# Performance work log

Measured on AMD Instinct MI355X. Metric: run time of the kernel, lower is better.

The kernel has to match this reference:

```python
import jax, jax.numpy as jnp
import numpy as np

B, S, H, NH = 4, 2048, 1024, 16
DK = H // NH


def setup_inputs() -> dict:
    key = jax.random.key(0)
    ks = jax.random.split(key, 12)
    sd = 1.0 / np.sqrt(H)
    inp = {
        "query": jax.random.normal(ks[0], (B, S, H), jnp.float32),
        "key_": jax.random.normal(ks[1], (B, S, H), jnp.float32),
        "value": jax.random.normal(ks[2], (B, S, H), jnp.float32),
        "mask": jax.random.randint(ks[3], (B, 1, S, S), 0, 2) == 1,
        "Wq": jax.random.uniform(ks[4], (H, H), jnp.float32, -sd, sd),
        "bq": jnp.zeros((H,), jnp.float32),
        "Wk": jax.random.uniform(ks[5], (H, H), jnp.float32, -sd, sd),
        "bk": jnp.zeros((H,), jnp.float32),
        "Wv": jax.random.uniform(ks[6], (H, H), jnp.float32, -sd, sd),
        "bv": jnp.zeros((H,), jnp.float32),
        "Wo": jax.random.uniform(ks[7], (H, H), jnp.float32, -sd, sd),
        "bo": jnp.zeros((H,), jnp.float32),
    }
    return inp


def reference(query, key_, value, mask, Wq, bq, Wk, bk, Wv, bv, Wo, bo):
    b = query.shape[0]
    # projections; nn.Linear computes x @ W^T + b
    q = (query @ Wq.T + bq).reshape(b, -1, NH, DK).transpose(0, 2, 1, 3)  # [B,NH,S,DK]
    k = (key_ @ Wk.T + bk).reshape(b, -1, NH, DK).transpose(0, 2, 1, 3)
    v = (value @ Wv.T + bv).reshape(b, -1, NH, DK).transpose(0, 2, 1, 3)
    scores = jnp.einsum("bhqd,bhkd->bhqk", q, k) / jnp.sqrt(jnp.float32(DK))
    min_val = jnp.finfo(scores.dtype).min
    scores = jnp.where(mask, min_val, scores)
    attn = jax.nn.softmax(scores, axis=-1)
    attn = jnp.where(mask, 0.0, attn)
    # dropout_rate = 0.0 -> identity
    x = jnp.einsum("bhqk,bhkd->bhqd", attn, v)
    x = x.transpose(0, 2, 1, 3).reshape(b, -1, NH * DK)  # [B,S,H]
    return x @ Wo.T + bo
```

## Files before the change

kernel.cpp:

```cpp
#include <hip/hip_runtime.h>
#include <hip/hip_bf16.h>
#include <stdint.h>

#define B_  4
#define S_  2048
#define H_  1024
#define NH_ 16
#define DK_ 64
#define M_  (B_*S_)

typedef unsigned short u16;
typedef __attribute__((ext_vector_type(8))) short bfrag;
typedef __attribute__((ext_vector_type(4))) float facc;
typedef __attribute__((ext_vector_type(16))) float f32x16;
typedef __attribute__((ext_vector_type(4))) unsigned int u32x4;
typedef __attribute__((ext_vector_type(2))) unsigned int u32x2;

__device__ __forceinline__ u16 f2bf(float f) {
  uint32_t u = __float_as_uint(f);
  return (u16)((u + 0x7fffu + ((u >> 16) & 1u)) >> 16);
}

__device__ __forceinline__ uint32_t cvtpk_bf16(float a, float b) {
  uint32_t r;
  asm("v_cvt_pk_bf16_f32 %0, %1, %2" : "=v"(r) : "v"(a), "v"(b));
  return r;
}

__global__ void cvt3_kernel(const float* __restrict__ a0, const float* __restrict__ a1,
                            const float* __restrict__ a2,
                            u16* __restrict__ o0, u16* __restrict__ o1, u16* __restrict__ o2,
                            int n4) {
  const float* in = blockIdx.y == 0 ? a0 : blockIdx.y == 1 ? a1 : a2;
  u16* out = blockIdx.y == 0 ? o0 : blockIdx.y == 1 ? o1 : o2;
  int i = blockIdx.x * blockDim.x + threadIdx.x;
  int stride = gridDim.x * blockDim.x;
  for (; i < n4; i += stride) {
    float4 v = reinterpret_cast<const float4*>(in)[i];
    ushort4 o;
    o.x = f2bf(v.x); o.y = f2bf(v.y); o.z = f2bf(v.z); o.w = f2bf(v.w);
    reinterpret_cast<ushort4*>(out)[i] = o;
  }
}

__global__ void cvt4_kernel(const float* __restrict__ a0, const float* __restrict__ a1,
                            const float* __restrict__ a2, const float* __restrict__ a3,
                            u16* __restrict__ o0, u16* __restrict__ o1,
                            u16* __restrict__ o2, u16* __restrict__ o3,
                            int n4, float s0) {
  int y = blockIdx.y;
  const float* in = y == 0 ? a0 : y == 1 ? a1 : y == 2 ? a2 : a3;
  u16* out = y == 0 ? o0 : y == 1 ? o1 : y == 2 ? o2 : o3;
  float sc = (y == 0) ? s0 : 1.0f;
  int i = blockIdx.x * blockDim.x + threadIdx.x;
  int stride = gridDim.x * blockDim.x;
  for (; i < n4; i += stride) {
    float4 v = reinterpret_cast<const float4*>(in)[i];
    ushort4 o;
    o.x = f2bf(v.x * sc); o.y = f2bf(v.y * sc);
    o.z = f2bf(v.z * sc); o.w = f2bf(v.w * sc);
    reinterpret_cast<ushort4*>(out)[i] = o;
  }
}

__global__ void pack_mask_kernel(const int* __restrict__ m, uint32_t* __restrict__ out) {
  int od = blockIdx.x * blockDim.x + threadIdx.x;
  int bq = od >> 9;
  int rem = od & 511;
  int c = rem >> 4, t = rem & 15;
  int hl = t >> 3, cc = (t >> 2) & 1, bb = t & 3;
  int4 v = *reinterpret_cast<const int4*>(m + (size_t)bq * 2048 + c*64 + 4*hl + 8*bb + 32*cc);
  uint32_t w = (v.x != 0 ? 1u : 0u) | (v.y != 0 ? 0x100u : 0u) |
               (v.z != 0 ? 0x10000u : 0u) | (v.w != 0 ? 0x1000000u : 0u);
  out[od] = w;
}

#define GLD16(gsrc, ldst) \
  __builtin_amdgcn_global_load_lds((const __attribute__((address_space(1))) void*)(gsrc), \
                                   (__attribute__((address_space(3))) void*)(ldst), 16, 0, 0)

__global__ __launch_bounds__(256) void qkv_gemm(const u16* __restrict__ qa, const u16* __restrict__ ka,
                                                const u16* __restrict__ va,
                                                const u16* __restrict__ Wqb, const u16* __restrict__ Wkb,
                                                const u16* __restrict__ Wvb,
                                                const float* __restrict__ bqp, const float* __restrict__ bkp,
                                                const float* __restrict__ bvp, float qbscale,
                                                u16* __restrict__ qh, u16* __restrict__ kh,
                                                u16* __restrict__ vt) {
  constexpr int K = H_;
  __shared__ __align__(16) u16 SH[2][128*32];
  u16* As = SH[0];
  u16* Bs = SH[1];
  const int tid = threadIdx.x;
  const int lane = tid & 63, wave = tid >> 6;
  const int lo = lane & 15, hi = lane >> 4;
  const int wr = wave >> 1, wc = wave & 1;
  const int wsel = blockIdx.y >> 3;
  const int m0 = blockIdx.x * 128, n0 = (blockIdx.y & 7) * 128;
  const u16* A  = wsel == 0 ? qa : wsel == 1 ? ka : va;
  const u16* Bm = wsel == 0 ? Wqb : wsel == 1 ? Wkb : Wvb;
  const float* bias = wsel == 0 ? bqp : wsel == 1 ? bkp : bvp;
  const float bscale = wsel == 0 ? qbscale : 1.0f;
  facc acc[4][4] = {};

  for (int k0 = 0; k0 < K; k0 += 32) {
    const u16* Ab = A + (size_t)m0 * K + k0;
    const u16* Bb = Bm + (size_t)n0 * K + k0;
    #pragma unroll
    for (int i = 0; i < 2; i++) {
      int idx = i*256 + tid;
      int row = idx >> 2, q = idx & 3;
      char* la = (char*)As + i*4096 + wave*1024;
      char* lb = (char*)Bs + i*4096 + wave*1024;
      GLD16(Ab + (size_t)row*K + q*8, la);
      GLD16(Bb + (size_t)row*K + q*8, lb);
    }
    __syncthreads();
    bfrag af[4], bfv[4];
    #pragma unroll
    for (int t = 0; t < 4; t++) {
      af[t]  = *reinterpret_cast<const bfrag*>(&As[(wr*64 + t*16 + lo)*32 + hi*8]);
      bfv[t] = *reinterpret_cast<const bfrag*>(&Bs[(wc*64 + t*16 + lo)*32 + hi*8]);
    }
    #pragma unroll
    for (int mt = 0; mt < 4; mt++)
      #pragma unroll
      for (int nt = 0; nt < 4; nt++)
        acc[mt][nt] = __builtin_amdgcn_mfma_f32_16x16x32_bf16(af[mt], bfv[nt], acc[mt][nt], 0, 0, 0);
    __syncthreads();
  }

  if (wsel < 2) {
    u16* o = wsel == 0 ? qh : kh;
    #pragma unroll
    for (int nt = 0; nt < 4; nt++) {
      int n = n0 + wc*64 + nt*16 + lo;
      float bv = bias[n] * bscale;
      int hh = n >> 6, d = n & 63;
      #pragma unroll
      for (int mt = 0; mt < 4; mt++) {
        #pragma unroll
        for (int r = 0; r < 4; r++) {
          int m = m0 + wr*64 + mt*16 + hi*4 + r;
          int bb = m >> 11, s = m & (S_ - 1);
          o[(((size_t)bb*NH_ + hh)*S_ + s)*DK_ + d] = f2bf(acc[mt][nt][r] + bv);
        }
      }
    }
  } else {
    u16* scr = &SH[0][0];
    const int bb2 = m0 >> 11, s0r = m0 & (S_ - 1);
    #pragma unroll
    for (int p = 0; p < 2; p++) {
      __syncthreads();
      if (wc == p) {
        #pragma unroll
        for (int nt = 0; nt < 4; nt++) {
          int d = nt*16 + lo;
          float bv = bias[n0 + p*64 + d];
          #pragma unroll
          for (int mt = 0; mt < 4; mt++) {
            #pragma unroll
            for (int r = 0; r < 4; r++) {
              int s = wr*64 + mt*16 + hi*4 + r;
              *(u16*)((char*)scr + d*256 + ((s*2) ^ ((d & 7) << 4))) = f2bf(acc[mt][nt][r] + bv);
            }
          }
        }
      }
      __syncthreads();
      int hh = (n0 >> 6) + p;
      u16* vbase = vt + ((size_t)bb2*NH_ + hh) * DK_ * S_ + s0r;
      #pragma unroll
      for (int i = 0; i < 4; i++) {
        int idx = i*256 + tid;
        int d = idx >> 4, sc = idx & 15;
        bfrag v = *reinterpret_cast<const bfrag*>((char*)scr + d*256 + ((sc*16) ^ ((d & 7) << 4)));
        *reinterpret_cast<bfrag*>(vbase + (size_t)d*S_ + sc*8) = v;
      }
    }
  }
}

__global__ __launch_bounds__(256) void gemm_out(const u16* __restrict__ A, const u16* __restrict__ Bm,
                                                const float* __restrict__ bias, float* __restrict__ o) {
  constexpr int K = H_, N = H_;
  __shared__ __align__(16) u16 As[128*32];
  __shared__ __align__(16) u16 Bs[128*32];
  const int tid = threadIdx.x;
  const int lane = tid & 63, wave = tid >> 6;
  const int lo = lane & 15, hi = lane >> 4;
  const int wr = wave >> 1, wc = wave & 1;
  const int m0 = blockIdx.x * 128, n0 = blockIdx.y * 128;
  facc acc[4][4] = {};

  for (int k0 = 0; k0 < K; k0 += 32) {
    const u16* Ab = A + (size_t)m0 * K + k0;
    const u16* Bb = Bm + (size_t)n0 * K + k0;
    #pragma unroll
    for (int i = 0; i < 2; i++) {
      int idx = i*256 + tid;
      int row = idx >> 2, q = idx & 3;
      char* la = (char*)As + i*4096 + wave*1024;
      char* lb = (char*)Bs + i*4096 + wave*1024;
      GLD16(Ab + (size_t)row*K + q*8, la);
      GLD16(Bb + (size_t)row*K + q*8, lb);
    }
    __syncthreads();
    bfrag af[4], bfv[4];
    #pragma unroll
    for (int t = 0; t < 4; t++) {
      af[t]  = *reinterpret_cast<const bfrag*>(&As[(wr*64 + t*16 + lo)*32 + hi*8]);
      bfv[t] = *reinterpret_cast<const bfrag*>(&Bs[(wc*64 + t*16 + lo)*32 + hi*8]);
    }
    #pragma unroll
    for (int mt = 0; mt < 4; mt++)
      #pragma unroll
      for (int nt = 0; nt < 4; nt++)
        acc[mt][nt] = __builtin_amdgcn_mfma_f32_16x16x32_bf16(af[mt], bfv[nt], acc[mt][nt], 0, 0, 0);
    __syncthreads();
  }

  #pragma unroll
  for (int nt = 0; nt < 4; nt++) {
    int n = n0 + wc*64 + nt*16 + lo;
    float bv = bias[n];
    #pragma unroll
    for (int mt = 0; mt < 4; mt++) {
      #pragma unroll
      for (int r = 0; r < 4; r++) {
        int m = m0 + wr*64 + mt*16 + hi*4 + r;
        o[(size_t)m*N + n] = acc[mt][nt][r] + bv;
      }
    }
  }
}

__global__ __launch_bounds__(256, 4) void attn_kernel(const u16* __restrict__ Qh, const u16* __restrict__ Kh,
                                                      const u16* __restrict__ Vt, const uint32_t* __restrict__ mbytes,
                                                      u16* __restrict__ xout) {
  __shared__ __align__(16) u16 Ks[2][64*64];
  __shared__ __align__(16) u16 Vs[2][64*64];
  const int tid = threadIdx.x;
  const int lane = tid & 63, wave = tid >> 6;
  const int l31 = lane & 31, hl = lane >> 5;
  const int gid = blockIdx.x;
  const int bh = (gid & 7) * 8 + (gid >> 7);
  const int qt = (gid >> 3) & 15;
  const int b = bh >> 4, hd = bh & 15;
  const int q0 = qt * 128;
  const size_t bhS = (size_t)bh * S_;
  const int swz = (lane & 7) << 4;

  bfrag qf[4];
  {
    const u16* qrow = Qh + (bhS + q0 + wave*32 + l31) * DK_;
    #pragma unroll
    for (int t = 0; t < 4; t++) qf[t] = *reinterpret_cast<const bfrag*>(qrow + t*16 + hl*8);
  }
  const char* mrowb = (const char*)mbytes + ((size_t)b * S_ + q0 + wave*32 + l31) * 2048 + hl*32;

  const int srow = wave*8 + (lane >> 3);
  const int scol = ((lane & 7) ^ (lane >> 3)) * 16;
  const char* ksrc = (const char*)(Kh + bhS * DK_) + (size_t)srow * 128 + scol;
  const char* vsrc = (const char*)(Vt + (size_t)bh * DK_ * S_) + (size_t)srow * (S_*2) + scol;

#define STAGE(buf, c) { \
    char* kl = (char*)Ks[buf] + wave*1024; \
    char* vl = (char*)Vs[buf] + wave*1024; \
    GLD16(ksrc + (size_t)(c)*8192,          kl); \
    GLD16(ksrc + (size_t)(c)*8192 + 4096,   kl + 4096); \
    GLD16(vsrc + (size_t)(c)*128,           vl); \
    GLD16(vsrc + (size_t)(c)*128 + 131072,  vl + 4096); \
  }

  float l_run = 0.f;
  f32x16 accO[2];
  #pragma unroll
  for (int e = 0; e < 16; e++) { accO[0][e] = 0.f; accO[1][e] = 0.f; }

  STAGE(0, 0);
  u32x4 mA_cur = *reinterpret_cast<const u32x4*>(mrowb);
  u32x4 mB_cur = *reinterpret_cast<const u32x4*>(mrowb + 16);
  __syncthreads();

  for (int c = 0; c < 32; c++) {
    const int cur = c & 1;
    if (c + 1 < 32) STAGE(cur ^ 1, c + 1);

    u32x4 mA = mA_cur, mB = mB_cur;
    if (c + 1 < 32) {
      mA_cur = *reinterpret_cast<const u32x4*>(mrowb + (c + 1)*64);
      mB_cur = *reinterpret_cast<const u32x4*>(mrowb + (c + 1)*64 + 16);
    }

    f32x16 s0, s1;
    #pragma unroll
    for (int r = 0; r < 16; r++) {
      float f0 = (float)((mA[r >> 2] >> ((r & 3) * 8)) & 0xffu);
      float f1 = (float)((mB[r >> 2] >> ((r & 3) * 8)) & 0xffu);
      s0[r] = __builtin_fmaf(f0, -1e36f, -8.0f);
      s1[r] = __builtin_fmaf(f1, -1e36f, -8.0f);
    }

    const char* KsB = (const char*)Ks[cur];
    __builtin_amdgcn_s_setprio(1);
    #pragma unroll
    for (int t = 0; t < 4; t++) {
      bfrag k0 = *reinterpret_cast<const bfrag*>(KsB + l31*128        + ((t*32 + hl*16) ^ swz));
      bfrag k1 = *reinterpret_cast<const bfrag*>(KsB + (32 + l31)*128 + ((t*32 + hl*16) ^ swz));
      s0 = __builtin_amdgcn_mfma_f32_32x32x16_bf16(k0, qf[t], s0, 0, 0, 0);
      s1 = __builtin_amdgcn_mfma_f32_32x32x16_bf16(k1, qf[t], s1, 0, 0, 0);
    }
    __builtin_amdgcn_s_setprio(0);

    #pragma unroll
    for (int r = 0; r < 16; r++) {
      s0[r] = __builtin_amdgcn_exp2f(s0[r]);
      s1[r] = __builtin_amdgcn_exp2f(s1[r]);
    }
    float a8[8];
    #pragma unroll
    for (int r = 0; r < 8; r++) a8[r] = (s0[r] + s0[r+8]) + (s1[r] + s1[r+8]);
    l_run += ((a8[0] + a8[1]) + (a8[2] + a8[3])) + ((a8[4] + a8[5]) + (a8[6] + a8[7]));

    u32x4 pa[4];
    #pragma unroll
    for (int kt = 0; kt < 2; kt++) {
      uint32_t W[8];
      #pragma unroll
      for (int j = 0; j < 8; j++)
        W[j] = kt == 0 ? cvtpk_bf16(s0[2*j], s0[2*j+1]) : cvtpk_bf16(s1[2*j], s1[2*j+1]);
      u32x2 r02 = __builtin_amdgcn_permlane32_swap(W[0], W[2], false, false);
      u32x2 r13 = __builtin_amdgcn_permlane32_swap(W[1], W[3], false, false);
      u32x2 r46 = __builtin_amdgcn_permlane32_swap(W[4], W[6], false, false);
      u32x2 r57 = __builtin_amdgcn_permlane32_swap(W[5], W[7], false, false);
      pa[kt*2    ][0] = r02[0]; pa[kt*2    ][1] = r13[0]; pa[kt*2    ][2] = r02[1]; pa[kt*2    ][3] = r13[1];
      pa[kt*2 + 1][0] = r46[0]; pa[kt*2 + 1][1] = r57[0]; pa[kt*2 + 1][2] = r46[1]; pa[kt*2 + 1][3] = r57[1];
    }

    const char* VsB = (const char*)Vs[cur];
    __builtin_amdgcn_s_setprio(1);
    #pragma unroll
    for (int ks = 0; ks < 4; ks++) {
      bfrag pb = __builtin_bit_cast(bfrag, pa[ks]);
      bfrag v0 = *reinterpret_cast<const bfrag*>(VsB + l31*128        + ((ks*32 + hl*16) ^ swz));
      bfrag v1 = *reinterpret_cast<const bfrag*>(VsB + (32 + l31)*128 + ((ks*32 + hl*16) ^ swz));
      accO[0] = __builtin_amdgcn_mfma_f32_32x32x16_bf16(v0, pb, accO[0], 0, 0, 0);
      accO[1] = __builtin_amdgcn_mfma_f32_32x32x16_bf16(v1, pb, accO[1], 0, 0, 0);
    }
    __builtin_amdgcn_s_setprio(0);
    __syncthreads();
  }
#undef STAGE

  float l_tot = l_run + __shfl_xor(l_run, 32);
  float linv = (l_tot > 0.f) ? (1.f / l_tot) : 0.f;
  u16* Xs = (u16*)Ks;
  {
    char* xb = (char*)Xs + (wave*32 + l31) * 128;
    #pragma unroll
    for (int dt = 0; dt < 2; dt++)
      #pragma unroll
      for (int j = 0; j < 8; j++) {
        uint32_t w = cvtpk_bf16(accO[dt][2*j] * linv, accO[dt][2*j+1] * linv);
        int d = dt*32 + ((2*j) & 3) + 8*((2*j) >> 2) + 4*hl;
        *reinterpret_cast<uint32_t*>(xb + ((d*2) ^ swz)) = w;
      }
  }
  __syncthreads();
  {
    int row = tid >> 1, d0 = (tid & 1) * 32;
    int rsw = (row & 7) << 4;
    u16* orow = xout + ((size_t)b * S_ + q0 + row) * H_ + hd * DK_ + d0;
    #pragma unroll
    for (int i = 0; i < 4; i++) {
      bfrag v = *reinterpret_cast<const bfrag*>((char*)Xs + row*128 + ((d0*2 + i*16) ^ rsw));
      *reinterpret_cast<bfrag*>((char*)orow + i*16) = v;
    }
  }
}

extern "C" void kernel_launch(void* const* d_in, const int* in_sizes, int n_in,
                              void* d_out, int out_size, void* d_ws, size_t ws_size,
                              hipStream_t stream) {
  const float* query = (const float*)d_in[0];
  const float* key_  = (const float*)d_in[1];
  const float* value = (const float*)d_in[2];
  const int*   mask  = (const int*)d_in[3];
  const float* Wq = (const float*)d_in[4];
  const float* bq = (const float*)d_in[5];
  const float* Wk = (const float*)d_in[6];
  const float* bk = (const float*)d_in[7];
  const float* Wv = (const float*)d_in[8];
  const float* bv = (const float*)d_in[9];
  const float* Wo = (const float*)d_in[10];
  const float* bo = (const float*)d_in[11];
  float* out = (float*)d_out;

  char* ws = (char*)d_ws;
  const size_t MB = 1024 * 1024;
  u16* q_act = (u16*)(ws + 0*MB);
  u16* k_act = (u16*)(ws + 16*MB);
  u16* v_act = (u16*)(ws + 32*MB);
  u16* wq_b  = (u16*)(ws + 48*MB);
  u16* wk_b  = (u16*)(ws + 50*MB);
  u16* wv_b  = (u16*)(ws + 52*MB);
  u16* wo_b  = (u16*)(ws + 54*MB);
  u16* qh    = (u16*)(ws + 56*MB);
  u16* kh    = (u16*)(ws + 72*MB);
  u16* vt    = (u16*)(ws + 104*MB);
  u16* xb    = (u16*)(ws + 120*MB);
  uint32_t* mbytes = (uint32_t*)(ws + 136*MB);

  const float QSCALE = 0.125f * 1.44269504088896f;

  const int nact4 = M_ * H_ / 4;
  cvt3_kernel<<<dim3(1024, 3), 256, 0, stream>>>(query, key_, value, q_act, k_act, v_act, nact4);
  const int nw4 = H_ * H_ / 4;
  cvt4_kernel<<<dim3(256, 4), 256, 0, stream>>>(Wq, Wk, Wv, Wo, wq_b, wk_b, wv_b, wo_b, nw4, QSCALE);
  const int ndwords = B_ * S_ * 512;
  pack_mask_kernel<<<ndwords/256, 256, 0, stream>>>(mask, mbytes);

  qkv_gemm<<<dim3(M_/128, 24), 256, 0, stream>>>(q_act, k_act, v_act, wq_b, wk_b, wv_b,
                                                 bq, bk, bv, QSCALE, qh, kh, vt);
  attn_kernel<<<1024, 256, 0, stream>>>(qh, kh, vt, mbytes, xb);
  gemm_out<<<dim3(M_/128, H_/128), 256, 0, stream>>>(xb, wo_b, bo, out);
}
```

Measured before the change: 240.6 us.

## Process 64 query rows per wave in attention to reuse K/V tiles

Each wave of the attention kernel now handles two 32-row query sub-tiles, so each block covers 256 query rows and the grid halves to 512 blocks. K fragments are loaded from LDS once per chunk and shared by both sub-tiles, and V fragments feed four MFMAs instead of two. This halves K/V global and LDS traffic per query row. In exchange, register use rises (launch bounds drop to 2 blocks per SM), which lowers occupancy and the number of blocks available to fill the GPU.

```diff
diff --git a/kernel.cpp b/kernel.cpp
--- a/kernel.cpp
+++ b/kernel.cpp
@@ -236,29 +236,31 @@
   }
 }
 
-__global__ __launch_bounds__(256, 4) void attn_kernel(const u16* __restrict__ Qh, const u16* __restrict__ Kh,
+__global__ __launch_bounds__(256, 2) void attn_kernel(const u16* __restrict__ Qh, const u16* __restrict__ Kh,
                                                       const u16* __restrict__ Vt, const uint32_t* __restrict__ mbytes,
                                                       u16* __restrict__ xout) {
-  __shared__ __align__(16) u16 Ks[2][64*64];
-  __shared__ __align__(16) u16 Vs[2][64*64];
+  __shared__ __align__(16) u16 SH[4][64*64];
   const int tid = threadIdx.x;
   const int lane = tid & 63, wave = tid >> 6;
   const int l31 = lane & 31, hl = lane >> 5;
   const int gid = blockIdx.x;
-  const int bh = (gid & 7) * 8 + (gid >> 7);
-  const int qt = (gid >> 3) & 15;
+  const int bh = (gid & 7) * 8 + ((gid >> 3) & 7);
+  const int qt = gid >> 6;
   const int b = bh >> 4, hd = bh & 15;
-  const int q0 = qt * 128;
+  const int q0 = qt * 256;
   const size_t bhS = (size_t)bh * S_;
   const int swz = (lane & 7) << 4;
-
-  bfrag qf[4];
-  {
-    const u16* qrow = Qh + (bhS + q0 + wave*32 + l31) * DK_;
-    #pragma unroll
-    for (int t = 0; t < 4; t++) qf[t] = *reinterpret_cast<const bfrag*>(qrow + t*16 + hl*8);
-  }
-  const char* mrowb = (const char*)mbytes + ((size_t)b * S_ + q0 + wave*32 + l31) * 2048 + hl*32;
+  const int qbase = q0 + wave*64;
+
+  bfrag qf[2][4];
+  #pragma unroll
+  for (int h = 0; h < 2; h++) {
+    const u16* qrow = Qh + (bhS + qbase + h*32 + l31) * DK_;
+    #pragma unroll
+    for (int t = 0; t < 4; t++) qf[h][t] = *reinterpret_cast<const bfrag*>(qrow + t*16 + hl*8);
+  }
+  const char* mrow0 = (const char*)mbytes + ((size_t)b * S_ + qbase + l31) * 2048 + hl*32;
+  const char* mrow1 = mrow0 + 32*2048;
 
   const int srow = wave*8 + (lane >> 3);
   const int scol = ((lane & 7) ^ (lane >> 3)) * 16;
@@ -266,117 +268,136 @@
   const char* vsrc = (const char*)(Vt + (size_t)bh * DK_ * S_) + (size_t)srow * (S_*2) + scol;
 
 #define STAGE(buf, c) { \
-    char* kl = (char*)Ks[buf] + wave*1024; \
-    char* vl = (char*)Vs[buf] + wave*1024; \
+    char* kl = (char*)SH[buf] + wave*1024; \
+    char* vl = (char*)SH[2 + (buf)] + wave*1024; \
     GLD16(ksrc + (size_t)(c)*8192,          kl); \
     GLD16(ksrc + (size_t)(c)*8192 + 4096,   kl + 4096); \
     GLD16(vsrc + (size_t)(c)*128,           vl); \
     GLD16(vsrc + (size_t)(c)*128 + 131072,  vl + 4096); \
   }
 
-  float l_run = 0.f;
-  f32x16 accO[2];
+  float l0 = 0.f, l1 = 0.f;
+  f32x16 accO[4];
   #pragma unroll
-  for (int e = 0; e < 16; e++) { accO[0][e] = 0.f; accO[1][e] = 0.f; }
+  for (int e = 0; e < 16; e++) { accO[0][e] = 0.f; accO[1][e] = 0.f; accO[2][e] = 0.f; accO[3][e] = 0.f; }
 
   STAGE(0, 0);
-  u32x4 mA_cur = *reinterpret_cast<const u32x4*>(mrowb);
-  u32x4 mB_cur = *reinterpret_cast<const u32x4*>(mrowb + 16);
+  u32x4 m0A_c = *reinterpret_cast<const u32x4*>(mrow0);
+  u32x4 m0B_c = *reinterpret_cast<const u32x4*>(mrow0 + 16);
+  u32x4 m1A_c = *reinterpret_cast<const u32x4*>(mrow1);
+  u32x4 m1B_c = *reinterpret_cast<const u32x4*>(mrow1 + 16);
   __syncthreads();
 
   for (int c = 0; c < 32; c++) {
     const int cur = c & 1;
     if (c + 1 < 32) STAGE(cur ^ 1, c + 1);
 
-    u32x4 mA = mA_cur, mB = mB_cur;
+    u32x4 m0A = m0A_c, m0B = m0B_c, m1A = m1A_c, m1B = m1B_c;
     if (c + 1 < 32) {
-      mA_cur = *reinterpret_cast<const u32x4*>(mrowb + (c + 1)*64);
-      mB_cur = *reinterpret_cast<const u32x4*>(mrowb + (c + 1)*64 + 16);
-    }
-
-    f32x16 s0, s1;
-    #pragma unroll
-    for (int r = 0; r < 16; r++) {
-      float f0 = (float)((mA[r >> 2] >> ((r & 3) * 8)) & 0xffu);
-      float f1 = (float)((mB[r >> 2] >> ((r & 3) * 8)) & 0xffu);
-      s0[r] = __builtin_fmaf(f0, -1e36f, -8.0f);
-      s1[r] = __builtin_fmaf(f1, -1e36f, -8.0f);
-    }
-
-    const char* KsB = (const char*)Ks[cur];
+      m0A_c = *reinterpret_cast<const u32x4*>(mrow0 + (c + 1)*64);
+      m0B_c = *reinterpret_cast<const u32x4*>(mrow0 + (c + 1)*64 + 16);
+      m1A_c = *reinterpret_cast<const u32x4*>(mrow1 + (c + 1)*64);
+      m1B_c = *reinterpret_cast<const u32x4*>(mrow1 + (c + 1)*64 + 16);
+    }
+
+    const char* KsB = (const char*)SH[cur];
+    bfrag kf[4][2];
+    #pragma unroll
+    for (int t = 0; t < 4; t++) {
+      kf[t][0] = *reinterpret_cast<const bfrag*>(KsB + l31*128        + ((t*32 + hl*16) ^ swz));
+      kf[t][1] = *reinterpret_cast<const bfrag*>(KsB + (32 + l31)*128 + ((t*32 + hl*16) ^ swz));
+    }
+
+    u32x4 pa0[4], pa1[4];
+    #pragma unroll
+    for (int h = 0; h < 2; h++) {
+      f32x16 s0, s1;
+      u32x4 mA = h ? m1A : m0A, mB = h ? m1B : m0B;
+      #pragma unroll
+      for (int r = 0; r < 16; r++) {
+        float f0 = (float)((mA[r >> 2] >> ((r & 3) * 8)) & 0xffu);
+        float f1 = (float)((mB[r >> 2] >> ((r & 3) * 8)) & 0xffu);
+        s0[r] = __builtin_fmaf(f0, -1e36f, -8.0f);
+        s1[r] = __builtin_fmaf(f1, -1e36f, -8.0f);
+      }
+      __builtin_amdgcn_s_setprio(1);
+      #pragma unroll
+      for (int t = 0; t < 4; t++) {
+        s0 = __builtin_amdgcn_mfma_f32_32x32x16_bf16(kf[t][0], qf[h][t], s0, 0, 0, 0);
+        s1 = __builtin_amdgcn_mfma_f32_32x32x16_bf16(kf[t][1], qf[h][t], s1, 0, 0, 0);
+      }
+      __builtin_amdgcn_s_setprio(0);
+      #pragma unroll
+      for (int r = 0; r < 16; r++) {
+        s0[r] = __builtin_amdgcn_exp2f(s0[r]);
+        s1[r] = __builtin_amdgcn_exp2f(s1[r]);
+      }
+      float a8[8];
+      #pragma unroll
+      for (int r = 0; r < 8; r++) a8[r] = (s0[r] + s0[r+8]) + (s1[r] + s1[r+8]);
+      float ls = ((a8[0] + a8[1]) + (a8[2] + a8[3])) + ((a8[4] + a8[5]) + (a8[6] + a8[7]));
+      if (h) l1 += ls; else l0 += ls;
+      #pragma unroll
+      for (int kt = 0; kt < 2; kt++) {
+        uint32_t W[8];
+        #pragma unroll
+        for (int j = 0; j < 8; j++)
+          W[j] = kt == 0 ? cvtpk_bf16(s0[2*j], s0[2*j+1]) : cvtpk_bf16(s1[2*j], s1[2*j+1]);
+        u32x2 r02 = __builtin_amdgcn_permlane32_swap(W[0], W[2], false, false);
+        u32x2 r13 = __builtin_amdgcn_permlane32_swap(W[1], W[3], false, false);
+        u32x2 r46 = __builtin_amdgcn_permlane32_swap(W[4], W[6], false, false);
+        u32x2 r57 = __builtin_amdgcn_permlane32_swap(W[5], W[7], false, false);
+        u32x4* pa = h ? pa1 : pa0;
+        pa[kt*2    ][0] = r02[0]; pa[kt*2    ][1] = r13[0]; pa[kt*2    ][2] = r02[1]; pa[kt*2    ][3] = r13[1];
+        pa[kt*2 + 1][0] = r46[0]; pa[kt*2 + 1][1] = r57[0]; pa[kt*2 + 1][2] = r46[1]; pa[kt*2 + 1][3] = r57[1];
+      }
+    }
+
+    const char* VsB = (const char*)SH[2 + cur];
     __builtin_amdgcn_s_setprio(1);
     #pragma unroll
-    for (int t = 0; t < 4; t++) {
-      bfrag k0 = *reinterpret_cast<const bfrag*>(KsB + l31*128        + ((t*32 + hl*16) ^ swz));
-      bfrag k1 = *reinterpret_cast<const bfrag*>(KsB + (32 + l31)*128 + ((t*32 + hl*16) ^ swz));
-      s0 = __builtin_amdgcn_mfma_f32_32x32x16_bf16(k0, qf[t], s0, 0, 0, 0);
-      s1 = __builtin_amdgcn_mfma_f32_32x32x16_bf16(k1, qf[t], s1, 0, 0, 0);
-    }
-    __builtin_amdgcn_s_setprio(0);
-
-    #pragma unroll
-    for (int r = 0; r < 16; r++) {
-      s0[r] = __builtin_amdgcn_exp2f(s0[r]);
-      s1[r] = __builtin_amdgcn_exp2f(s1[r]);
-    }
-    float a8[8];
-    #pragma unroll
-    for (int r = 0; r < 8; r++) a8[r] = (s0[r] + s0[r+8]) + (s1[r] + s1[r+8]);
-    l_run += ((a8[0] + a8[1]) + (a8[2] + a8[3])) + ((a8[4] + a8[5]) + (a8[6] + a8[7]));
-
-    u32x4 pa[4];
-    #pragma unroll
-    for (int kt = 0; kt < 2; kt++) {
-      uint32_t W[8];
-      #pragma unroll
-      for (int j = 0; j < 8; j++)
-        W[j] = kt == 0 ? cvtpk_bf16(s0[2*j], s0[2*j+1]) : cvtpk_bf16(s1[2*j], s1[2*j+1]);
-      u32x2 r02 = __builtin_amdgcn_permlane32_swap(W[0], W[2], false, false);
-      u32x2 r13 = __builtin_amdgcn_permlane32_swap(W[1], W[3], false, false);
-      u32x2 r46 = __builtin_amdgcn_permlane32_swap(W[4], W[6], false, false);
-      u32x2 r57 = __builtin_amdgcn_permlane32_swap(W[5], W[7], false, false);
-      pa[kt*2    ][0] = r02[0]; pa[kt*2    ][1] = r13[0]; pa[kt*2    ][2] = r02[1]; pa[kt*2    ][3] = r13[1];
-      pa[kt*2 + 1][0] = r46[0]; pa[kt*2 + 1][1] = r57[0]; pa[kt*2 + 1][2] = r46[1]; pa[kt*2 + 1][3] = r57[1];
-    }
-
-    const char* VsB = (const char*)Vs[cur];
-    __builtin_amdgcn_s_setprio(1);
-    #pragma unroll
     for (int ks = 0; ks < 4; ks++) {
-      bfrag pb = __builtin_bit_cast(bfrag, pa[ks]);
       bfrag v0 = *reinterpret_cast<const bfrag*>(VsB + l31*128        + ((ks*32 + hl*16) ^ swz));
       bfrag v1 = *reinterpret_cast<const bfrag*>(VsB + (32 + l31)*128 + ((ks*32 + hl*16) ^ swz));
-      accO[0] = __builtin_amdgcn_mfma_f32_32x32x16_bf16(v0, pb, accO[0], 0, 0, 0);
-      accO[1] = __builtin_amdgcn_mfma_f32_32x32x16_bf16(v1, pb, accO[1], 0, 0, 0);
+      bfrag pb0 = __builtin_bit_cast(bfrag, pa0[ks]);
+      bfrag pb1 = __builtin_bit_cast(bfrag, pa1[ks]);
+      accO[0] = __builtin_amdgcn_mfma_f32_32x32x16_bf16(v0, pb0, accO[0], 0, 0, 0);
+      accO[1] = __builtin_amdgcn_mfma_f32_32x32x16_bf16(v1, pb0, accO[1], 0, 0, 0);
+      accO[2] = __builtin_amdgcn_mfma_f32_32x32x16_bf16(v0, pb1, accO[2], 0, 0, 0);
+      accO[3] = __builtin_amdgcn_mfma_f32_32x32x16_bf16(v1, pb1, accO[3], 0, 0, 0);
     }
     __builtin_amdgcn_s_setprio(0);
     __syncthreads();
   }
 #undef STAGE
 
-  float l_tot = l_run + __shfl_xor(l_run, 32);
-  float linv = (l_tot > 0.f) ? (1.f / l_tot) : 0.f;
-  u16* Xs = (u16*)Ks;
-  {
-    char* xb = (char*)Xs + (wave*32 + l31) * 128;
+  float lt0 = l0 + __shfl_xor(l0, 32);
+  float lt1 = l1 + __shfl_xor(l1, 32);
+  float li[2];
+  li[0] = (lt0 > 0.f) ? (1.f / lt0) : 0.f;
+  li[1] = (lt1 > 0.f) ? (1.f / lt1) : 0.f;
+  u16* Xs = (u16*)SH;
+  #pragma unroll
+  for (int h = 0; h < 2; h++) {
+    char* xb = (char*)Xs + (wave*64 + h*32 + l31) * 128;
     #pragma unroll
     for (int dt = 0; dt < 2; dt++)
       #pragma unroll
       for (int j = 0; j < 8; j++) {
-        uint32_t w = cvtpk_bf16(accO[dt][2*j] * linv, accO[dt][2*j+1] * linv);
+        uint32_t w = cvtpk_bf16(accO[h*2 + dt][2*j] * li[h], accO[h*2 + dt][2*j+1] * li[h]);
         int d = dt*32 + ((2*j) & 3) + 8*((2*j) >> 2) + 4*hl;
         *reinterpret_cast<uint32_t*>(xb + ((d*2) ^ swz)) = w;
       }
   }
   __syncthreads();
   {
-    int row = tid >> 1, d0 = (tid & 1) * 32;
+    int row = tid;
     int rsw = (row & 7) << 4;
-    u16* orow = xout + ((size_t)b * S_ + q0 + row) * H_ + hd * DK_ + d0;
-    #pragma unroll
-    for (int i = 0; i < 4; i++) {
-      bfrag v = *reinterpret_cast<const bfrag*>((char*)Xs + row*128 + ((d0*2 + i*16) ^ rsw));
-      *reinterpret_cast<bfrag*>((char*)orow + i*16) = v;
+    u16* orow = xout + ((size_t)b * S_ + q0 + row) * H_ + hd * DK_;
+    #pragma unroll
+    for (int i = 0; i < 8; i++) {
+      bfrag v = *reinterpret_cast<const bfrag*>((char*)Xs + row*128 + ((i*16) ^ rsw));
+      *reinterpret_cast<bfrag*>(orow + i*8) = v;
     }
   }
 }
@@ -424,6 +445,6 @@
 
   qkv_gemm<<<dim3(M_/128, 24), 256, 0, stream>>>(q_act, k_act, v_act, wq_b, wk_b, wv_b,
                                                  bq, bk, bv, QSCALE, qh, kh, vt);
-  attn_kernel<<<1024, 256, 0, stream>>>(qh, kh, vt, mbytes, xb);
+  attn_kernel<<<512, 256, 0, stream>>>(qh, kh, vt, mbytes, xb);
   gemm_out<<<dim3(M_/128, H_/128), 256, 0, stream>>>(xb, wo_b, bo, out);
 }
```

Measured after the change: 271.2 us. 1.13x slower.
